# Kernel optimization log

Hardware: AMD Instinct MI355X
Metric: run time of the kernel (lower is better)

The kernel has to match this reference:

```python
import jax, jax.numpy as jnp
import numpy as np

N_NODES = 50000
N_EDGES = 500000
IN_DIM = 512
HID = 512


def setup_inputs() -> dict:
    key = jax.random.key(0)
    ks = jax.random.split(key, 12)
    s = 0.02  # weight init scale
    x = jax.random.normal(ks[0], (N_NODES, IN_DIM), dtype=jnp.float32)
    edge_index = jax.random.randint(ks[1], (2, N_EDGES), 0, N_NODES, dtype=jnp.int32)
    return {
        "x": x,
        "edge_index": edge_index,
        "Wl0": jax.random.normal(ks[2], (IN_DIM, HID), jnp.float32) * s,
        "bl0": jnp.zeros((HID,), jnp.float32),
        "Wr0": jax.random.normal(ks[3], (IN_DIM, HID), jnp.float32) * s,
        "Wl1": jax.random.normal(ks[4], (HID, HID), jnp.float32) * s,
        "bl1": jnp.zeros((HID,), jnp.float32),
        "Wr1": jax.random.normal(ks[5], (HID, HID), jnp.float32) * s,
        "Wv": jax.random.normal(ks[6], (HID, HID), jnp.float32) * s,
        "bv": jnp.zeros((HID,), jnp.float32),
        "Wt": jax.random.normal(ks[7], (HID, HID), jnp.float32) * s,
        "bt": jnp.zeros((HID,), jnp.float32),
    }


def _sage_conv(x, src, dst, Wl, bl, Wr, n_nodes):
    # mean-aggregate source features at target nodes, then dual linear
    msg_sum = jax.ops.segment_sum(x[src], dst, num_segments=n_nodes)  # [N, d]
    deg = jax.ops.segment_sum(jnp.ones_like(dst, dtype=x.dtype), dst, num_segments=n_nodes)
    mean = msg_sum / jnp.maximum(deg, 1.0)[:, None]
    return mean @ Wl + bl + x @ Wr


def reference(x, edge_index, Wl0, bl0, Wr0, Wl1, bl1, Wr1, Wv, bv, Wt, bt):
    n = x.shape[0]
    src, dst = edge_index[0], edge_index[1]
    h = _sage_conv(x, src, dst, Wl0, bl0, Wr0, n)
    h = jax.nn.relu(h)  # dropout is identity in eval mode
    h = _sage_conv(h, src, dst, Wl1, bl1, Wr1, n)
    x_vision = jax.nn.relu(h @ Wv + bv)
    x_text = jax.nn.relu(h @ Wt + bt)
    return (h, x_vision, x_text)
```

## Files before the change

kernel.cpp:

```cpp
#include <hip/hip_runtime.h>
#include <hip/hip_bf16.h>
#include <stdint.h>

#define N_NODES 50000
#define N_EDGES 500000
#define DIM 512

typedef unsigned short u16;
typedef unsigned int u32;
typedef __bf16 bf16x8 __attribute__((ext_vector_type(8)));
typedef float f32x4 __attribute__((ext_vector_type(4)));

static __device__ __forceinline__ u16 f2bf(float f) {
  union { __bf16 b; u16 u; } cv; cv.b = (__bf16)f; return cv.u;
}
static __device__ __forceinline__ float bf2f(u16 u) {
  union { u16 u; __bf16 b; } cv; cv.u = u; return (float)cv.b;
}

__global__ __launch_bounds__(1024) void k_scan(const int* __restrict__ deg,
                                               int* __restrict__ offs,
                                               int* __restrict__ pos,
                                               float* __restrict__ invd) {
  __shared__ int sums[1024];
  const int tid = threadIdx.x;
  const int CH = 49;
  int lo = tid * CH;
  int hi = lo + CH; if (hi > N_NODES) hi = N_NODES;
  if (lo > N_NODES) lo = N_NODES;
  int s = 0;
  for (int i = lo; i < hi; ++i) s += deg[i];
  sums[tid] = s;
  __syncthreads();
  for (int off = 1; off < 1024; off <<= 1) {
    int t = (tid >= off) ? sums[tid - off] : 0;
    __syncthreads();
    sums[tid] += t;
    __syncthreads();
  }
  int run = sums[tid] - s;
  for (int i = lo; i < hi; ++i) {
    int d = deg[i];
    offs[i] = run; pos[i] = run;
    invd[i] = 1.0f / (float)((d > 1) ? d : 1);
    run += d;
  }
  if (tid == 1023) offs[N_NODES] = run;
}

__global__ void k_scatter(const int* __restrict__ src, const int* __restrict__ dst,
                          int* __restrict__ pos, int* __restrict__ srcs) {
  int e = blockIdx.x * blockDim.x + threadIdx.x;
  if (e < N_EDGES) {
    int p = atomicAdd(&pos[dst[e]], 1);
    srcs[p] = src[e] * DIM;
  }
}

__global__ __launch_bounds__(256) void k_prep(
    const float* __restrict__ x, u16* __restrict__ xb,
    const int* __restrict__ dst, int* __restrict__ deg,
    const float* __restrict__ Wa, const float* __restrict__ Wb,
    const float* __restrict__ Wc, const float* __restrict__ Wd,
    const float* __restrict__ We, const float* __restrict__ Wf,
    u16* __restrict__ Oa, u16* __restrict__ Ob, u16* __restrict__ Oc,
    u16* __restrict__ Od, u16* __restrict__ Oe, u16* __restrict__ Of) {
  __shared__ u16 tbuf[64][66];
  const int t = blockIdx.x * 256 + threadIdx.x;

  const float4* p = (const float4*)(x + (size_t)t * 8);
  float4 a = p[0], b = p[1];
  uint4 o;
  o.x = (u32)f2bf(a.x) | ((u32)f2bf(a.y) << 16);
  o.y = (u32)f2bf(a.z) | ((u32)f2bf(a.w) << 16);
  o.z = (u32)f2bf(b.x) | ((u32)f2bf(b.y) << 16);
  o.w = (u32)f2bf(b.z) | ((u32)f2bf(b.w) << 16);
  *(uint4*)(xb + (size_t)t * 8) = o;

  if (t < N_EDGES) atomicAdd(&deg[dst[t]], 1);

  const int wb = (int)blockIdx.x - (12500 - 384);
  if (wb >= 0) {
    const float* W; u16* O;
    switch (wb / 64) {
      case 0: W = Wa; O = Oa; break;
      case 1: W = Wb; O = Ob; break;
      case 2: W = Wc; O = Oc; break;
      case 3: W = Wd; O = Od; break;
      case 4: W = We; O = Oe; break;
      default: W = Wf; O = Of; break;
    }
    const int rem = wb & 63;
    const int k0 = (rem & 7) * 64, n0 = (rem >> 3) * 64;
    const int lr = threadIdx.x & 63, wr = threadIdx.x >> 6;
#pragma unroll
    for (int rr = 0; rr < 16; ++rr) {
      int k = k0 + wr * 16 + rr;
      tbuf[lr][wr * 16 + rr] = f2bf(W[(size_t)k * 512 + n0 + lr]);
    }
    __syncthreads();
#pragma unroll
    for (int rr = 0; rr < 16; ++rr) {
      int n = n0 + wr * 16 + rr;
      O[(size_t)n * 512 + k0 + lr] = tbuf[wr * 16 + rr][lr];
    }
  }
}

#define ACC1(q)                                              \
  acc[0] += bf2f((q).x & 0xffff); acc[1] += bf2f((u16)((q).x >> 16)); \
  acc[2] += bf2f((q).y & 0xffff); acc[3] += bf2f((u16)((q).y >> 16)); \
  acc[4] += bf2f((q).z & 0xffff); acc[5] += bf2f((u16)((q).z >> 16)); \
  acc[6] += bf2f((q).w & 0xffff); acc[7] += bf2f((u16)((q).w >> 16));

__global__ __launch_bounds__(256) void k_agg_bf16(
    const u16* __restrict__ hb, const int* __restrict__ offs,
    const int* __restrict__ srcs, const float* __restrict__ invd,
    u16* __restrict__ outb) {
  int node = blockIdx.x * 4 + (threadIdx.x >> 6);
  int lane = threadIdx.x & 63;
  if (node >= N_NODES) return;
  int s0 = offs[node], s1 = offs[node + 1];
  float acc[8] = {0, 0, 0, 0, 0, 0, 0, 0};
  const u16* hl = hb + lane * 8;
  int i = s0;
  for (; i + 4 <= s1; i += 4) {
    int sa = srcs[i], sb = srcs[i + 1], sc = srcs[i + 2], sd = srcs[i + 3];
    uint4 qa = *(const uint4*)(hl + sa);
    uint4 qb = *(const uint4*)(hl + sb);
    uint4 qc = *(const uint4*)(hl + sc);
    uint4 qd = *(const uint4*)(hl + sd);
    ACC1(qa) ACC1(qb) ACC1(qc) ACC1(qd)
  }
  if (i + 2 <= s1) {
    int sa = srcs[i], sb = srcs[i + 1];
    uint4 qa = *(const uint4*)(hl + sa);
    uint4 qb = *(const uint4*)(hl + sb);
    ACC1(qa) ACC1(qb)
    i += 2;
  }
  if (i < s1) {
    int sa = srcs[i];
    uint4 qa = *(const uint4*)(hl + sa);
    ACC1(qa)
  }
  float iv = invd[node];
  uint4 o;
  o.x = (u32)f2bf(acc[0] * iv) | ((u32)f2bf(acc[1] * iv) << 16);
  o.y = (u32)f2bf(acc[2] * iv) | ((u32)f2bf(acc[3] * iv) << 16);
  o.z = (u32)f2bf(acc[4] * iv) | ((u32)f2bf(acc[5] * iv) << 16);
  o.w = (u32)f2bf(acc[6] * iv) | ((u32)f2bf(acc[7] * iv) << 16);
  *(uint4*)(outb + (size_t)node * DIM + lane * 8) = o;
}

#define MFMA __builtin_amdgcn_mfma_f32_16x16x32_bf16

template <int EPI>
__global__ __launch_bounds__(512, 2) void k_gemm8(
    const u16* __restrict__ A1, const u16* __restrict__ W1,
    const u16* __restrict__ A2, const u16* __restrict__ W2,
    const float* __restrict__ bias, const float* __restrict__ bias2,
    float* __restrict__ outf, float* __restrict__ outf2,
    u16* __restrict__ outb, int NT) {
  __shared__ u16 lds[4 * 16384];
  const int tid = threadIdx.x;
  const int wid = tid >> 6, lane = tid & 63;
  const int wm = wid >> 2, wn = wid & 3;
  int head = 0, row0, colb;
  if (EPI == 3) {
    head = ((int)blockIdx.x >> 1) & 1;
    colb = ((int)blockIdx.x & 1) * 256;
    row0 = ((int)blockIdx.x >> 2) * 256;
  } else {
    row0 = ((int)blockIdx.x >> 1) * 256;
    colb = ((int)blockIdx.x & 1) * 256;
  }
  const u16* Bsrc = (EPI == 3) ? (head ? W2 : W1) : nullptr;

  f32x4 acc[8][4];
  const f32x4 z = {0.f, 0.f, 0.f, 0.f};
#pragma unroll
  for (int i = 0; i < 8; ++i)
#pragma unroll
    for (int j = 0; j < 4; ++j) acc[i][j] = z;

  const int lx = lane & 7, ly = lane >> 3;
  const int schunk = lx ^ ly;

  auto stage = [&](int t, int isB, int h) {
    u16* tile = lds + (size_t)(((t & 1) << 1) + isB) * 16384;
    const u16* G;
    if (EPI == 3) G = isB ? Bsrc : A1;
    else G = (t < 8) ? (isB ? W1 : A1) : (isB ? W2 : A2);
    const int kofs = ((t & 7) * 64) + schunk * 8;
    const int r0 = isB ? colb : row0;
#pragma unroll
    for (int q = 0; q < 2; ++q) {
      const int srw = q * 64 + wid * 8;
      const int r_w = ((srw >> 4) << 5) + h * 16 + (srw & 15);
      int rg = r0 + r_w + ly;
      if (!isB && rg > N_NODES - 1) rg = N_NODES - 1;
      const u16* g = G + (size_t)rg * 512 + kofs;
      __builtin_amdgcn_global_load_lds(
          (const __attribute__((address_space(1))) void*)g,
          (__attribute__((address_space(3))) void*)(tile + r_w * 64), 16, 0, 0);
    }
  };

  auto rdA = [&](const u16* T_, int ig, int kk) -> bf16x8 {
    const int r = (wm * 8 + ig) * 16 + (lane & 15);
    const int off = ((kk * 4 + (lane >> 4)) ^ (lane & 7)) * 8;
    return *(const bf16x8*)(T_ + r * 64 + off);
  };
  auto rdB = [&](const u16* T_, int jg, int kk) -> bf16x8 {
    const int r = (wn * 4 + jg) * 16 + (lane & 15);
    const int off = ((kk * 4 + (lane >> 4)) ^ (lane & 7)) * 8;
    return *(const bf16x8*)(T_ + r * 64 + off);
  };

  stage(0, 0, 0); stage(0, 1, 0); stage(0, 0, 1); stage(0, 1, 1);

  for (int t = 0; t < NT; ++t) {
    const u16* At = lds + (size_t)((t & 1) << 1) * 16384;
    const u16* Bt = At + 16384;
    const bool more = (t + 1 < NT);
    bf16x8 aF[4][2], bF[2][2];

    asm volatile("s_waitcnt vmcnt(4)" ::: "memory");
    __builtin_amdgcn_s_barrier();
    asm volatile("" ::: "memory");
    if (more) stage(t + 1, 0, 0);
#pragma unroll
    for (int ip = 0; ip < 4; ++ip)
#pragma unroll
      for (int kk = 0; kk < 2; ++kk) aF[ip][kk] = rdA(At, 2 * ip, kk);
#pragma unroll
    for (int jp = 0; jp < 2; ++jp)
#pragma unroll
      for (int kk = 0; kk < 2; ++kk) bF[jp][kk] = rdB(Bt, 2 * jp, kk);
    __builtin_amdgcn_s_setprio(1);
#pragma unroll
    for (int ip = 0; ip < 4; ++ip)
#pragma unroll
      for (int jp = 0; jp < 2; ++jp)
#pragma unroll
        for (int kk = 0; kk < 2; ++kk)
          acc[2 * ip][2 * jp] = MFMA(aF[ip][kk], bF[jp][kk], acc[2 * ip][2 * jp], 0, 0, 0);
    __builtin_amdgcn_s_setprio(0);

    if (more) { asm volatile("s_waitcnt vmcnt(2)" ::: "memory"); }
    else      { asm volatile("s_waitcnt vmcnt(0)" ::: "memory"); }
    __builtin_amdgcn_s_barrier();
    asm volatile("" ::: "memory");
    if (more) stage(t + 1, 1, 0);
#pragma unroll
    for (int jp = 0; jp < 2; ++jp)
#pragma unroll
      for (int kk = 0; kk < 2; ++kk) bF[jp][kk] = rdB(Bt, 2 * jp + 1, kk);
    __builtin_amdgcn_s_setprio(1);
#pragma unroll
    for (int ip = 0; ip < 4; ++ip)
#pragma unroll
      for (int jp = 0; jp < 2; ++jp)
#pragma unroll
        for (int kk = 0; kk < 2; ++kk)
          acc[2 * ip][2 * jp + 1] = MFMA(aF[ip][kk], bF[jp][kk], acc[2 * ip][2 * jp + 1], 0, 0, 0);
    __builtin_amdgcn_s_setprio(0);

    if (more) stage(t + 1, 0, 1);
#pragma unroll
    for (int ip = 0; ip < 4; ++ip)
#pragma unroll
      for (int kk = 0; kk < 2; ++kk) aF[ip][kk] = rdA(At, 2 * ip + 1, kk);
    __builtin_amdgcn_s_setprio(1);
#pragma unroll
    for (int ip = 0; ip < 4; ++ip)
#pragma unroll
      for (int jp = 0; jp < 2; ++jp)
#pragma unroll
        for (int kk = 0; kk < 2; ++kk)
          acc[2 * ip + 1][2 * jp + 1] = MFMA(aF[ip][kk], bF[jp][kk], acc[2 * ip + 1][2 * jp + 1], 0, 0, 0);
    __builtin_amdgcn_s_setprio(0);

    if (more) stage(t + 1, 1, 1);
#pragma unroll
    for (int jp = 0; jp < 2; ++jp)
#pragma unroll
      for (int kk = 0; kk < 2; ++kk) bF[jp][kk] = rdB(Bt, 2 * jp, kk);
    __builtin_amdgcn_s_setprio(1);
#pragma unroll
    for (int ip = 0; ip < 4; ++ip)
#pragma unroll
      for (int jp = 0; jp < 2; ++jp)
#pragma unroll
        for (int kk = 0; kk < 2; ++kk)
          acc[2 * ip + 1][2 * jp] = MFMA(aF[ip][kk], bF[jp][kk], acc[2 * ip + 1][2 * jp], 0, 0, 0);
    __builtin_amdgcn_s_setprio(0);
  }

  const float* bs = (EPI == 3 && head) ? bias2 : bias;
  float* of = (EPI == 3 && head) ? outf2 : outf;
#pragma unroll
  for (int jg = 0; jg < 4; ++jg) {
    int col = colb + (wn * 4 + jg) * 16 + (lane & 15);
    float bb = bs[col];
#pragma unroll
    for (int ig = 0; ig < 8; ++ig) {
      int rbase = row0 + (wm * 8 + ig) * 16 + (lane >> 4) * 4;
      f32x4 v = acc[ig][jg];
#pragma unroll
      for (int r = 0; r < 4; ++r) {
        int row = rbase + r;
        if (row < N_NODES) {
          float f = v[r] + bb;
          if (EPI == 0) {
            f = fmaxf(f, 0.f);
            outb[(size_t)row * DIM + col] = f2bf(f);
          } else if (EPI == 1) {
            outf[(size_t)row * DIM + col] = f;
            outb[(size_t)row * DIM + col] = f2bf(f);
          } else {
            of[(size_t)row * DIM + col] = fmaxf(f, 0.f);
          }
        }
      }
    }
  }
}

extern "C" void kernel_launch(void* const* d_in, const int* in_sizes, int n_in,
                              void* d_out, int out_size, void* d_ws, size_t ws_size,
                              hipStream_t stream) {
  (void)in_sizes; (void)n_in; (void)out_size; (void)ws_size;
  const float* x   = (const float*)d_in[0];
  const int*   ei  = (const int*)d_in[1];
  const float* Wl0 = (const float*)d_in[2];
  const float* bl0 = (const float*)d_in[3];
  const float* Wr0 = (const float*)d_in[4];
  const float* Wl1 = (const float*)d_in[5];
  const float* bl1 = (const float*)d_in[6];
  const float* Wr1 = (const float*)d_in[7];
  const float* Wv  = (const float*)d_in[8];
  const float* bv  = (const float*)d_in[9];
  const float* Wt  = (const float*)d_in[10];
  const float* bt  = (const float*)d_in[11];
  const int* srcI = ei;
  const int* dstI = ei + N_EDGES;

  float* out_h = (float*)d_out;
  float* out_v = out_h + (size_t)N_NODES * DIM;
  float* out_t = out_v + (size_t)N_NODES * DIM;
  u16* meanb  = (u16*)out_v;
  u16* hrelub = (u16*)out_t;

  uint8_t* p = (uint8_t*)d_ws;
  auto carve = [&](size_t bytes) -> uint8_t* {
    uint8_t* r = p; p += (bytes + 1023) & ~(size_t)1023; return r;
  };
  int*   deg  = (int*)carve((size_t)N_NODES * 4);
  int*   offs = (int*)carve((size_t)(N_NODES + 1) * 4);
  int*   pos  = (int*)carve((size_t)N_NODES * 4);
  float* invd = (float*)carve((size_t)N_NODES * 4);
  int*   srcs = (int*)carve((size_t)N_EDGES * 4);
  u16* Wl0b = (u16*)carve(512 * 512 * 2);
  u16* Wr0b = (u16*)carve(512 * 512 * 2);
  u16* Wl1b = (u16*)carve(512 * 512 * 2);
  u16* Wr1b = (u16*)carve(512 * 512 * 2);
  u16* Wvb  = (u16*)carve(512 * 512 * 2);
  u16* Wtb  = (u16*)carve(512 * 512 * 2);
  u16* xb   = (u16*)carve((size_t)N_NODES * DIM * 2);

  const int EB = (N_EDGES + 255) / 256;

  hipMemsetAsync(deg, 0, (size_t)N_NODES * 4, stream);

  k_prep<<<12500, 256, 0, stream>>>(x, xb, dstI, deg,
                                    Wl0, Wr0, Wl1, Wr1, Wv, Wt,
                                    Wl0b, Wr0b, Wl1b, Wr1b, Wvb, Wtb);
  k_scan<<<1, 1024, 0, stream>>>(deg, offs, pos, invd);
  k_scatter<<<EB, 256, 0, stream>>>(srcI, dstI, pos, srcs);

  const int GB = 392;

  k_agg_bf16<<<12500, 256, 0, stream>>>(xb, offs, srcs, invd, meanb);
  k_gemm8<0><<<GB, 512, 0, stream>>>(meanb, Wl0b, xb, Wr0b, bl0, nullptr,
                                     nullptr, nullptr, hrelub, 16);

  k_agg_bf16<<<12500, 256, 0, stream>>>(hrelub, offs, srcs, invd, meanb);
  k_gemm8<1><<<GB, 512, 0, stream>>>(meanb, Wl1b, hrelub, Wr1b, bl1, nullptr,
                                     out_h, nullptr, xb, 16);

  k_gemm8<3><<<784, 512, 0, stream>>>(xb, Wvb, nullptr, Wtb, bv, bt,
                                      out_v, out_t, nullptr, 8);
}
```

Baseline: 668.4 us.

## Retile GEMMs to 112-row by full-width 512-column blocks

Replaces the 256x256 output tile with a 112x512 tile, so each block covers the full output width. Every wave now owns 64 columns across all 112 rows, and the A and B staging and the wait counts are rewritten to match. The goal is to read each A row once instead of twice and to fit 448 blocks, close to a whole multiple of the CU count, instead of 392. In exchange, each block streams the full 512-row weight slice per k-step, which raises per-block B traffic and LDS use (about 160KB for two buffers), and 7 row groups map awkwardly onto 4-wide fragment passes.

```diff
diff --git a/kernel.cpp b/kernel.cpp
--- a/kernel.cpp
+++ b/kernel.cpp
@@ -154,90 +154,96 @@
 }
 
 #define MFMA __builtin_amdgcn_mfma_f32_16x16x32_bf16
+#define BUFU 39936
 
 template <int EPI>
-__global__ __launch_bounds__(512, 2) void k_gemm8(
+__global__ __launch_bounds__(512, 2) void k_gemm112(
     const u16* __restrict__ A1, const u16* __restrict__ W1,
     const u16* __restrict__ A2, const u16* __restrict__ W2,
     const float* __restrict__ bias, const float* __restrict__ bias2,
     float* __restrict__ outf, float* __restrict__ outf2,
     u16* __restrict__ outb, int NT) {
-  __shared__ u16 lds[4 * 16384];
+  __shared__ u16 lds[2 * BUFU];
   const int tid = threadIdx.x;
   const int wid = tid >> 6, lane = tid & 63;
-  const int wm = wid >> 2, wn = wid & 3;
-  int head = 0, row0, colb;
+  int head = 0, row0;
   if (EPI == 3) {
-    head = ((int)blockIdx.x >> 1) & 1;
-    colb = ((int)blockIdx.x & 1) * 256;
-    row0 = ((int)blockIdx.x >> 2) * 256;
+    head = (int)blockIdx.x & 1;
+    row0 = ((int)blockIdx.x >> 1) * 112;
   } else {
-    row0 = ((int)blockIdx.x >> 1) * 256;
-    colb = ((int)blockIdx.x & 1) * 256;
-  }
-  const u16* Bsrc = (EPI == 3) ? (head ? W2 : W1) : nullptr;
-
-  f32x4 acc[8][4];
+    row0 = (int)blockIdx.x * 112;
+  }
+  const u16* BW = (EPI == 3) ? (head ? W2 : W1) : nullptr;
+
+  f32x4 acc[7][4];
   const f32x4 z = {0.f, 0.f, 0.f, 0.f};
 #pragma unroll
-  for (int i = 0; i < 8; ++i)
+  for (int i = 0; i < 7; ++i)
 #pragma unroll
     for (int j = 0; j < 4; ++j) acc[i][j] = z;
 
-  const int lx = lane & 7, ly = lane >> 3;
-  const int schunk = lx ^ ly;
-
-  auto stage = [&](int t, int isB, int h) {
-    u16* tile = lds + (size_t)(((t & 1) << 1) + isB) * 16384;
-    const u16* G;
-    if (EPI == 3) G = isB ? Bsrc : A1;
-    else G = (t < 8) ? (isB ? W1 : A1) : (isB ? W2 : A2);
-    const int kofs = ((t & 7) * 64) + schunk * 8;
-    const int r0 = isB ? colb : row0;
-#pragma unroll
-    for (int q = 0; q < 2; ++q) {
-      const int srw = q * 64 + wid * 8;
-      const int r_w = ((srw >> 4) << 5) + h * 16 + (srw & 15);
-      int rg = r0 + r_w + ly;
-      if (!isB && rg > N_NODES - 1) rg = N_NODES - 1;
-      const u16* g = G + (size_t)rg * 512 + kofs;
+  const int ly = lane >> 3;
+  const int schunk = (lane & 7) ^ ly;
+
+  auto stageA = [&](int t, int h) {
+    u16* tile = lds + (t & 1) * BUFU;
+    const u16* G = (EPI == 3) ? A1 : ((t < 8) ? A1 : A2);
+    int w = wid;
+    if (h && w >= 6) w -= 2;
+    const int rb = h * 64 + w * 8;
+    int rg = row0 + rb + ly;
+    if (rg > N_NODES - 1) rg = N_NODES - 1;
+    const u16* g = G + (size_t)rg * 512 + (t & 7) * 64 + schunk * 8;
+    __builtin_amdgcn_global_load_lds(
+        (const __attribute__((address_space(1))) void*)g,
+        (__attribute__((address_space(3))) void*)(tile + rb * 64), 16, 0, 0);
+  };
+
+  auto stageB = [&](int t, int jh) {
+    u16* tile = lds + (t & 1) * BUFU + 7168;
+    const u16* G = (EPI == 3) ? BW : ((t < 8) ? W1 : W2);
+    const int kofs = (t & 7) * 64 + schunk * 8;
+#pragma unroll
+    for (int u = 0; u < 4; ++u) {
+      const int rb = u * 128 + (wid >> 2) * 64 + (wid & 3) * 8 + jh * 32;
+      const u16* g = G + (size_t)(rb + ly) * 512 + kofs;
       __builtin_amdgcn_global_load_lds(
           (const __attribute__((address_space(1))) void*)g,
-          (__attribute__((address_space(3))) void*)(tile + r_w * 64), 16, 0, 0);
+          (__attribute__((address_space(3))) void*)(tile + rb * 64), 16, 0, 0);
     }
   };
 
   auto rdA = [&](const u16* T_, int ig, int kk) -> bf16x8 {
-    const int r = (wm * 8 + ig) * 16 + (lane & 15);
+    const int r = ig * 16 + (lane & 15);
     const int off = ((kk * 4 + (lane >> 4)) ^ (lane & 7)) * 8;
     return *(const bf16x8*)(T_ + r * 64 + off);
   };
   auto rdB = [&](const u16* T_, int jg, int kk) -> bf16x8 {
-    const int r = (wn * 4 + jg) * 16 + (lane & 15);
+    const int r = wid * 64 + jg * 16 + (lane & 15);
     const int off = ((kk * 4 + (lane >> 4)) ^ (lane & 7)) * 8;
     return *(const bf16x8*)(T_ + r * 64 + off);
   };
 
-  stage(0, 0, 0); stage(0, 1, 0); stage(0, 0, 1); stage(0, 1, 1);
+  stageA(0, 0); stageB(0, 0); stageB(0, 1); stageA(0, 1);
 
   for (int t = 0; t < NT; ++t) {
-    const u16* At = lds + (size_t)((t & 1) << 1) * 16384;
-    const u16* Bt = At + 16384;
+    const u16* At = lds + (t & 1) * BUFU;
+    const u16* Bt = At + 7168;
     const bool more = (t + 1 < NT);
     bf16x8 aF[4][2], bF[2][2];
 
-    asm volatile("s_waitcnt vmcnt(4)" ::: "memory");
+    asm volatile("s_waitcnt vmcnt(5)" ::: "memory");
     __builtin_amdgcn_s_barrier();
     asm volatile("" ::: "memory");
-    if (more) stage(t + 1, 0, 0);
+    if (more) stageA(t + 1, 0);
 #pragma unroll
     for (int ip = 0; ip < 4; ++ip)
 #pragma unroll
-      for (int kk = 0; kk < 2; ++kk) aF[ip][kk] = rdA(At, 2 * ip, kk);
+      for (int kk = 0; kk < 2; ++kk) aF[ip][kk] = rdA(At, ip, kk);
 #pragma unroll
     for (int jp = 0; jp < 2; ++jp)
 #pragma unroll
-      for (int kk = 0; kk < 2; ++kk) bF[jp][kk] = rdB(Bt, 2 * jp, kk);
+      for (int kk = 0; kk < 2; ++kk) bF[jp][kk] = rdB(Bt, jp, kk);
     __builtin_amdgcn_s_setprio(1);
 #pragma unroll
     for (int ip = 0; ip < 4; ++ip)
@@ -245,18 +251,18 @@
       for (int jp = 0; jp < 2; ++jp)
 #pragma unroll
         for (int kk = 0; kk < 2; ++kk)
-          acc[2 * ip][2 * jp] = MFMA(aF[ip][kk], bF[jp][kk], acc[2 * ip][2 * jp], 0, 0, 0);
+          acc[ip][jp] = MFMA(aF[ip][kk], bF[jp][kk], acc[ip][jp], 0, 0, 0);
     __builtin_amdgcn_s_setprio(0);
 
-    if (more) { asm volatile("s_waitcnt vmcnt(2)" ::: "memory"); }
+    if (more) { asm volatile("s_waitcnt vmcnt(1)" ::: "memory"); }
     else      { asm volatile("s_waitcnt vmcnt(0)" ::: "memory"); }
     __builtin_amdgcn_s_barrier();
     asm volatile("" ::: "memory");
-    if (more) stage(t + 1, 1, 0);
+    if (more) stageB(t + 1, 0);
 #pragma unroll
     for (int jp = 0; jp < 2; ++jp)
 #pragma unroll
-      for (int kk = 0; kk < 2; ++kk) bF[jp][kk] = rdB(Bt, 2 * jp + 1, kk);
+      for (int kk = 0; kk < 2; ++kk) bF[jp][kk] = rdB(Bt, 2 + jp, kk);
     __builtin_amdgcn_s_setprio(1);
 #pragma unroll
     for (int ip = 0; ip < 4; ++ip)
@@ -264,37 +270,37 @@
       for (int jp = 0; jp < 2; ++jp)
 #pragma unroll
         for (int kk = 0; kk < 2; ++kk)
-          acc[2 * ip][2 * jp + 1] = MFMA(aF[ip][kk], bF[jp][kk], acc[2 * ip][2 * jp + 1], 0, 0, 0);
+          acc[ip][2 + jp] = MFMA(aF[ip][kk], bF[jp][kk], acc[ip][2 + jp], 0, 0, 0);
     __builtin_amdgcn_s_setprio(0);
 
-    if (more) stage(t + 1, 0, 1);
-#pragma unroll
-    for (int ip = 0; ip < 4; ++ip)
-#pragma unroll
-      for (int kk = 0; kk < 2; ++kk) aF[ip][kk] = rdA(At, 2 * ip + 1, kk);
+    if (more) stageB(t + 1, 1);
+#pragma unroll
+    for (int ip = 0; ip < 3; ++ip)
+#pragma unroll
+      for (int kk = 0; kk < 2; ++kk) aF[ip][kk] = rdA(At, 4 + ip, kk);
     __builtin_amdgcn_s_setprio(1);
 #pragma unroll
-    for (int ip = 0; ip < 4; ++ip)
+    for (int ip = 0; ip < 3; ++ip)
 #pragma unroll
       for (int jp = 0; jp < 2; ++jp)
 #pragma unroll
         for (int kk = 0; kk < 2; ++kk)
-          acc[2 * ip + 1][2 * jp + 1] = MFMA(aF[ip][kk], bF[jp][kk], acc[2 * ip + 1][2 * jp + 1], 0, 0, 0);
+          acc[4 + ip][2 + jp] = MFMA(aF[ip][kk], bF[jp][kk], acc[4 + ip][2 + jp], 0, 0, 0);
     __builtin_amdgcn_s_setprio(0);
 
-    if (more) stage(t + 1, 1, 1);
+    if (more) stageA(t + 1, 1);
 #pragma unroll
     for (int jp = 0; jp < 2; ++jp)
 #pragma unroll
-      for (int kk = 0; kk < 2; ++kk) bF[jp][kk] = rdB(Bt, 2 * jp, kk);
+      for (int kk = 0; kk < 2; ++kk) bF[jp][kk] = rdB(Bt, jp, kk);
     __builtin_amdgcn_s_setprio(1);
 #pragma unroll
-    for (int ip = 0; ip < 4; ++ip)
+    for (int ip = 0; ip < 3; ++ip)
 #pragma unroll
       for (int jp = 0; jp < 2; ++jp)
 #pragma unroll
         for (int kk = 0; kk < 2; ++kk)
-          acc[2 * ip + 1][2 * jp] = MFMA(aF[ip][kk], bF[jp][kk], acc[2 * ip + 1][2 * jp], 0, 0, 0);
+          acc[4 + ip][jp] = MFMA(aF[ip][kk], bF[jp][kk], acc[4 + ip][jp], 0, 0, 0);
     __builtin_amdgcn_s_setprio(0);
   }
 
@@ -302,11 +308,11 @@
   float* of = (EPI == 3 && head) ? outf2 : outf;
 #pragma unroll
   for (int jg = 0; jg < 4; ++jg) {
-    int col = colb + (wn * 4 + jg) * 16 + (lane & 15);
+    int col = wid * 64 + jg * 16 + (lane & 15);
     float bb = bs[col];
 #pragma unroll
-    for (int ig = 0; ig < 8; ++ig) {
-      int rbase = row0 + (wm * 8 + ig) * 16 + (lane >> 4) * 4;
+    for (int ig = 0; ig < 7; ++ig) {
+      int rbase = row0 + ig * 16 + (lane >> 4) * 4;
       f32x4 v = acc[ig][jg];
 #pragma unroll
       for (int r = 0; r < 4; ++r) {
@@ -380,16 +386,16 @@
   k_scan<<<1, 1024, 0, stream>>>(deg, offs, pos, invd);
   k_scatter<<<EB, 256, 0, stream>>>(srcI, dstI, pos, srcs);
 
-  const int GB = 392;
+  const int GB = 448;
 
   k_agg_bf16<<<12500, 256, 0, stream>>>(xb, offs, srcs, invd, meanb);
-  k_gemm8<0><<<GB, 512, 0, stream>>>(meanb, Wl0b, xb, Wr0b, bl0, nullptr,
-                                     nullptr, nullptr, hrelub, 16);
+  k_gemm112<0><<<GB, 512, 0, stream>>>(meanb, Wl0b, xb, Wr0b, bl0, nullptr,
+                                       nullptr, nullptr, hrelub, 16);
 
   k_agg_bf16<<<12500, 256, 0, stream>>>(hrelub, offs, srcs, invd, meanb);
-  k_gemm8<1><<<GB, 512, 0, stream>>>(meanb, Wl1b, hrelub, Wr1b, bl1, nullptr,
-                                     out_h, nullptr, xb, 16);
-
-  k_gemm8<3><<<784, 512, 0, stream>>>(xb, Wvb, nullptr, Wtb, bv, bt,
-                                      out_v, out_t, nullptr, 8);
-}
+  k_gemm112<1><<<GB, 512, 0, stream>>>(meanb, Wl1b, hrelub, Wr1b, bl1, nullptr,
+                                       out_h, nullptr, xb, 16);
+
+  k_gemm112<3><<<896, 512, 0, stream>>>(xb, Wvb, nullptr, Wtb, bv, bt,
+                                        out_v, out_t, nullptr, 8);
+}
```

Result: faster. 650.8 us (-2.6%).
